# Kernel optimization log

Hardware: AMD Instinct MI355X
Metric: run time of the kernel (lower is better)

## Reference

```python
import jax, jax.numpy as jnp
import numpy as np

T, DM = 2048, 2048
H, KV, D = 16, 2, 128
E, I_MOE, I_SH = 16, 768, 768
TOP_K, N_GROUP, TOPK_GROUP = 4, 4, 2
ROPE_THETA = 1e6
EPS = 1e-5
ROUTED_SCALE = 1.0


def rmsnorm(x, w):
    v = jnp.mean(x * x, axis=-1, keepdims=True)
    return x * jax.lax.rsqrt(v + EPS) * w


def apply_rope(x, pos):
    # partial rotary: first D//2 dims rotated (neox style), rest passthrough
    rd = D // 2
    half = rd // 2
    inv = 1.0 / (ROPE_THETA ** (jnp.arange(0, rd, 2, dtype=jnp.float32) / rd))
    freqs = pos.astype(jnp.float32)[:, None] * inv  # [T, half]
    cos = jnp.cos(freqs)[:, None, :]
    sin = jnp.sin(freqs)[:, None, :]
    x1, x2 = x[..., :half], x[..., half:rd]
    rot = jnp.concatenate([x1 * cos - x2 * sin, x2 * cos + x1 * sin], axis=-1)
    return jnp.concatenate([rot, x[..., rd:]], axis=-1)


def mlp(x, wgu, wd):
    g, u = jnp.split(x @ wgu, 2, axis=-1)
    return (jax.nn.silu(g) * u) @ wd


def attention(x, pos, w_qkv, b_qkv, w_o, q_norm_w, k_norm_w):
    qkv = x @ w_qkv + b_qkv
    q, k, v = jnp.split(qkv, [H * D, H * D + KV * D], axis=-1)
    q = rmsnorm(q.reshape(T, H, D), q_norm_w)
    k = rmsnorm(k.reshape(T, KV, D), k_norm_w)
    v = v.reshape(T, KV, D)
    q = apply_rope(q, pos)
    k = apply_rope(k, pos)
    rep = H // KV
    k = jnp.repeat(k, rep, axis=1)
    v = jnp.repeat(v, rep, axis=1)
    scores = jnp.einsum('thd,shd->hts', q, k) * (D ** -0.5)
    causal = pos[:, None] >= pos[None, :]
    scores = jnp.where(causal[None], scores, jnp.finfo(scores.dtype).min)
    p = jax.nn.softmax(scores, axis=-1)
    o = jnp.einsum('hts,shd->thd', p, v).reshape(T, H * D)
    return o @ w_o


def moe(x, gate_w, gate_bias, shared_wgu, shared_wd, expert_wgu, expert_wd):
    # sigmoid grouped top-k routing with e_score_correction_bias (DeepSeek/GLM style)
    logits = x.astype(jnp.float32) @ gate_w
    scores = jax.nn.sigmoid(logits)
    sb = scores + gate_bias
    g = sb.reshape(T, N_GROUP, E // N_GROUP)
    group_scores = jnp.sum(jax.lax.top_k(g, 2)[0], axis=-1)  # [T, n_group]
    _, gi = jax.lax.top_k(group_scores, TOPK_GROUP)
    gmask = jnp.zeros((T, N_GROUP)).at[jnp.arange(T)[:, None], gi].set(1.0)
    emask = jnp.repeat(gmask, E // N_GROUP, axis=1)
    masked = jnp.where(emask > 0, sb, -jnp.inf)
    _, idx = jax.lax.top_k(masked, TOP_K)  # [T, top_k]
    w = jnp.take_along_axis(scores, idx, axis=1)
    w = w / jnp.sum(w, axis=1, keepdims=True)  # renormalize (norm_topk_prob)
    cw = jnp.zeros((T, E)).at[jnp.arange(T)[:, None], idx].add(w)  # dense combine weights
    gu = jnp.einsum('td,edi->tei', x, expert_wgu)  # [T, E, 2I]
    gt, ut = jnp.split(gu, 2, axis=-1)
    act = jax.nn.silu(gt) * ut * cw[:, :, None]
    routed = jnp.einsum('tei,eid->td', act, expert_wd)
    shared = mlp(x, shared_wgu, shared_wd)
    return routed * ROUTED_SCALE + shared


def setup_inputs() -> dict:
    key = jax.random.key(0)
    ks = jax.random.split(key, 12)
    s = 0.02
    return {
        'positions': jnp.arange(T, dtype=jnp.int32),
        'hidden_states': jax.random.normal(ks[0], (T, DM), jnp.float32),
        'residual': jax.random.normal(ks[1], (T, DM), jnp.float32),
        'ln1_w': jnp.ones((DM,), jnp.float32),
        'ln2_w': jnp.ones((DM,), jnp.float32),
        'w_qkv': jax.random.normal(ks[2], (DM, (H + 2 * KV) * D), jnp.float32) * s,
        'b_qkv': jnp.zeros(((H + 2 * KV) * D,), jnp.float32),
        'w_o': jax.random.normal(ks[3], (H * D, DM), jnp.float32) * s,
        'q_norm_w': jnp.ones((D,), jnp.float32),
        'k_norm_w': jnp.ones((D,), jnp.float32),
        'gate_w': jax.random.normal(ks[4], (DM, E), jnp.float32) * s,
        'gate_bias': jax.random.normal(ks[5], (E,), jnp.float32) * 0.1,
        'shared_wgu': jax.random.normal(ks[6], (DM, 2 * I_SH), jnp.float32) * s,
        'shared_wd': jax.random.normal(ks[7], (I_SH, DM), jnp.float32) * s,
        'expert_wgu': jax.random.normal(ks[8], (E, DM, 2 * I_MOE), jnp.float32) * s,
        'expert_wd': jax.random.normal(ks[9], (E, I_MOE, DM), jnp.float32) * s,
    }


def reference(positions, hidden_states, residual, ln1_w, ln2_w, w_qkv, b_qkv, w_o,
              q_norm_w, k_norm_w, gate_w, gate_bias, shared_wgu, shared_wd,
              expert_wgu, expert_wd):
    # fused add + RMSNorm (residual is not None path)
    residual = hidden_states + residual
    h = rmsnorm(residual, ln1_w)
    h = attention(h, positions, w_qkv, b_qkv, w_o, q_norm_w, k_norm_w)
    residual = h + residual
    h = rmsnorm(residual, ln2_w)
    h = moe(h, gate_w, gate_bias, shared_wgu, shared_wd, expert_wgu, expert_wd)
    return h, residual
```

## Files before the change

### kernel.cpp

```cpp
#include <hip/hip_runtime.h>
#include <stdint.h>
#include <math.h>

#define T_ 2048
#define DM 2048
#define NH 16
#define NKV 2
#define HD 128
#define QKVN 2560
#define NE 16
#define IM 768
#define ISH 768
#define MAXROWS 10240
#define ROWS_ALL 12288
#define NBLK 136
#define SM_SCALE 0.08838834764831845f

typedef __attribute__((ext_vector_type(8))) short short8;
typedef __attribute__((ext_vector_type(4))) float f32x4;

__device__ __forceinline__ float bf2f(unsigned short u){ return __uint_as_float(((unsigned int)u)<<16); }
__device__ __forceinline__ unsigned short f2bf(float f){
  unsigned int u = __float_as_uint(f);
  return (unsigned short)((u + 0x7FFFu + ((u>>16)&1u)) >> 16);
}
__device__ __forceinline__ void split2(float x, unsigned short& hi, unsigned short& lo){
  hi = f2bf(x);
  lo = f2bf(x - bf2f(hi));
}

__device__ __forceinline__ void gload16(const void* g, void* l){
  __builtin_amdgcn_global_load_lds((const __attribute__((address_space(1))) unsigned int*)g,
                                   (__attribute__((address_space(3))) unsigned int*)l, 16, 0, 0);
}

__device__ __forceinline__ int xcd_swz(int bid, int nwg){
  int q = nwg >> 3, r = nwg & 7, x = bid & 7, p = bid >> 3;
  return (x < r ? x*(q+1) : r*(q+1) + (x-r)*q) + p;
}

#define BAR()    asm volatile("s_barrier" ::: "memory")
#define VW(N)    asm volatile("s_waitcnt vmcnt(" #N ")" ::: "memory")
#define LW0()    do{ asm volatile("s_waitcnt lgkmcnt(0)" ::: "memory"); __builtin_amdgcn_sched_barrier(0); }while(0)

template<bool ILV>
__global__ void k_tconv(const float* __restrict__ src, unsigned short* __restrict__ dst,
                        const float* __restrict__ srcS, unsigned short* __restrict__ dstS,
                        int R, int C, size_t sS, size_t sD){
  int z = blockIdx.z;
  if (srcS && z == gridDim.z-1){ src = srcS; dst = dstS; }
  else { src += (size_t)z * sS; dst += (size_t)z * sD; }
  __shared__ float tile[64*65];
  int tid = threadIdx.x;
  int r0 = blockIdx.y*64, c0 = blockIdx.x*64;
  int lr = tid>>4, lc = (tid&15)*4;
  #pragma unroll
  for (int j=0;j<4;j++){
    int row = j*16 + lr;
    float4 v = *(const float4*)&src[(size_t)(r0+row)*C + c0 + lc];
    float* t = &tile[row*65 + lc];
    t[0]=v.x; t[1]=v.y; t[2]=v.z; t[3]=v.w;
  }
  __syncthreads();
  #pragma unroll
  for (int jj=0;jj<2;jj++){
    int slot = jj*256 + tid;
    int c = slot>>3, ro = (slot&7)*8;
    int cg = c0 + c;
    int cd = cg;
    if (ILV){ int b = cg>>3, inner = cg&7; cd = (b<96 ? b*16 : (b-96)*16+8) + inner; }
    short8 o;
    #pragma unroll
    for (int k=0;k<8;k++) o[k] = (short)f2bf(tile[(ro+k)*65 + c]);
    *(short8*)&dst[(size_t)cd*R + r0 + ro] = o;
  }
}

__global__ void k_tconv2(const float* __restrict__ src, unsigned short* __restrict__ dhi,
                         unsigned short* __restrict__ dlo, int R, int C){
  __shared__ float tile[64*65];
  int tid = threadIdx.x;
  int r0 = blockIdx.y*64, c0 = blockIdx.x*64;
  int lr = tid>>4, lc = (tid&15)*4;
  #pragma unroll
  for (int j=0;j<4;j++){
    int row = j*16 + lr;
    float4 v = *(const float4*)&src[(size_t)(r0+row)*C + c0 + lc];
    float* t = &tile[row*65 + lc];
    t[0]=v.x; t[1]=v.y; t[2]=v.z; t[3]=v.w;
  }
  __syncthreads();
  #pragma unroll
  for (int jj=0;jj<2;jj++){
    int slot = jj*256 + tid;
    int c = slot>>3, ro = (slot&7)*8;
    short8 oh, ol;
    #pragma unroll
    for (int k=0;k<8;k++){
      unsigned short h_, l_;
      split2(tile[(ro+k)*65 + c], h_, l_);
      oh[k] = (short)h_; ol[k] = (short)l_;
    }
    size_t o = (size_t)(c0+c)*R + r0 + ro;
    *(short8*)&dhi[o] = oh;
    *(short8*)&dlo[o] = ol;
  }
}

template<bool ROUTE>
__global__ void k_add_rmsnorm(const float* __restrict__ a, const float* __restrict__ b,
                              const float* __restrict__ w, float* __restrict__ resout,
                              unsigned short* __restrict__ ohi, unsigned short* __restrict__ olo,
                              unsigned short* __restrict__ obf,
                              const float* __restrict__ gw, const float* __restrict__ gbias,
                              int* __restrict__ idx4, float* __restrict__ w4){
  int t = blockIdx.x, tid = threadIdx.x;
  const float4* a4 = (const float4*)(a + (size_t)t*DM);
  const float4* b4 = (const float4*)(b + (size_t)t*DM);
  float4 va = a4[tid], vb = b4[tid];
  float4 wa = a4[tid+256], wb = b4[tid+256];
  float4 v0, v1;
  v0.x=va.x+vb.x; v0.y=va.y+vb.y; v0.z=va.z+vb.z; v0.w=va.w+vb.w;
  v1.x=wa.x+wb.x; v1.y=wa.y+wb.y; v1.z=wa.z+wb.z; v1.w=wa.w+wb.w;
  float s = v0.x*v0.x+v0.y*v0.y+v0.z*v0.z+v0.w*v0.w
          + v1.x*v1.x+v1.y*v1.y+v1.z*v1.z+v1.w*v1.w;
  #pragma unroll
  for (int o=32;o;o>>=1) s += __shfl_xor(s,o);
  __shared__ float sm[4];
  if ((tid&63)==0) sm[tid>>6]=s;
  __syncthreads();
  s = sm[0]+sm[1]+sm[2]+sm[3];
  float rs = rsqrtf(s*(1.f/(float)DM) + 1e-5f);
  ((float4*)(resout + (size_t)t*DM))[tid] = v0;
  ((float4*)(resout + (size_t)t*DM))[tid+256] = v1;
  const float4* w4p_ = (const float4*)w;
  float4 w0 = w4p_[tid], w1 = w4p_[tid+256];
  float n[8] = { v0.x*rs*w0.x, v0.y*rs*w0.y, v0.z*rs*w0.z, v0.w*rs*w0.w,
                 v1.x*rs*w1.x, v1.y*rs*w1.y, v1.z*rs*w1.z, v1.w*rs*w1.w };
  if (ohi){
    ushort4 h0,h1,l0,l1;
    split2(n[0],h0.x,l0.x); split2(n[1],h0.y,l0.y); split2(n[2],h0.z,l0.z); split2(n[3],h0.w,l0.w);
    split2(n[4],h1.x,l1.x); split2(n[5],h1.y,l1.y); split2(n[6],h1.z,l1.z); split2(n[7],h1.w,l1.w);
    ((ushort4*)(ohi + (size_t)t*DM))[tid] = h0;
    ((ushort4*)(ohi + (size_t)t*DM))[tid+256] = h1;
    ((ushort4*)(olo + (size_t)t*DM))[tid] = l0;
    ((ushort4*)(olo + (size_t)t*DM))[tid+256] = l1;
  }
  if (obf){
    ushort4 o0 = make_ushort4(f2bf(n[0]),f2bf(n[1]),f2bf(n[2]),f2bf(n[3]));
    ushort4 o1 = make_ushort4(f2bf(n[4]),f2bf(n[5]),f2bf(n[6]),f2bf(n[7]));
    ((ushort4*)(obf + (size_t)t*DM))[tid] = o0;
    ((ushort4*)(obf + (size_t)t*DM))[tid+256] = o1;
  }
  if constexpr (ROUTE){
    __shared__ float xrow[DM];
    __shared__ float red[16][17];
    #pragma unroll
    for (int jj=0;jj<4;jj++) xrow[4*tid+jj] = n[jj];
    #pragma unroll
    for (int jj=0;jj<4;jj++) xrow[1024+4*tid+jj] = n[4+jj];
    __syncthreads();
    int e = tid & 15, grp = tid >> 4;
    float part = 0.f;
    #pragma unroll 8
    for (int c = grp; c < DM; c += 16)
      part += xrow[c] * gw[(size_t)c*16 + e];
    red[grp][e] = part;
    __syncthreads();
    if (tid==0){
      float sc[16], sb[16];
      for (int ee=0;ee<16;ee++){
        float lg = 0.f;
        for (int g2=0;g2<16;g2++) lg += red[g2][ee];
        sc[ee] = 1.f/(1.f+expf(-lg));
        sb[ee] = sc[ee] + gbias[ee];
      }
      float gs[4];
      for (int g=0;g<4;g++){
        float m1=-3.4e38f, m2=-3.4e38f;
        for (int j=0;j<4;j++){
          float v = sb[g*4+j];
          if (v>m1){ m2=m1; m1=v; } else if (v>m2) m2=v;
        }
        gs[g]=m1+m2;
      }
      int g1=0; for (int g=1;g<4;g++) if (gs[g]>gs[g1]) g1=g;
      int g2=-1; for (int g=0;g<4;g++){ if (g==g1) continue; if (g2<0 || gs[g]>gs[g2]) g2=g; }
      float msk[16];
      for (int ee=0;ee<16;ee++){ int g=ee>>2; msk[ee] = (g==g1||g==g2)? sb[ee] : -3.4e38f; }
      int id[4]; float wv[4]; float wsum=0.f;
      for (int s2=0;s2<4;s2++){
        int bb=0; float bv=-3.5e38f;
        for (int ee=0;ee<16;ee++) if (msk[ee]>bv){ bv=msk[ee]; bb=ee; }
        id[s2]=bb; wv[s2]=sc[bb]; wsum+=sc[bb]; msk[bb]=-3.5e38f;
      }
      float invs = 1.f/wsum;
      for (int s2=0;s2<4;s2++){
        idx4[t*4+s2]=id[s2];
        w4[t*4+s2]=wv[s2]*invs;
      }
    }
  }
}

template<bool GATHER, bool ACT>
__global__ __launch_bounds__(256) void k_gemm2(
    const unsigned short* __restrict__ A, const unsigned short* __restrict__ Be,
    const unsigned short* __restrict__ Bsh, unsigned short* __restrict__ C,
    int K, int lda, int ldb, int ldc,
    const int* __restrict__ offs, size_t sBe, const int* __restrict__ tok){
  int nx = gridDim.x;
  int nwg = nx * gridDim.y;
  int wid_ = xcd_swz(blockIdx.x + nx*blockIdx.y, nwg);
  int tN = wid_ % nx, tM = wid_ / nx;
  int rb = tM*128;
  if (rb >= offs[17]) return;
  const unsigned short* B;
  if (rb >= offs[16]) B = Bsh;
  else {
    int e=0;
    for (; e<15; ++e) if (offs[e+1] > rb) break;
    B = Be + (size_t)e*sBe;
  }
  __shared__ __align__(16) unsigned short As[2][4096];
  __shared__ __align__(16) unsigned short Bs[2][4096];
  int tid = threadIdx.x, lane = tid & 63, wwid = tid >> 6;
  int wr = wwid >> 1, wc = wwid & 1;
  const unsigned short* Bb = B + (size_t)tN*128*ldb;

  const unsigned short* Asrc0;
  const unsigned short* Asrc1;
  int r0s = tid>>2, r1s = r0s + 64;
  {
    if (GATHER){
      Asrc0 = A + (size_t)tok[rb + r0s]*lda;
      Asrc1 = A + (size_t)tok[rb + r1s]*lda;
    } else {
      Asrc0 = A + (size_t)(rb + r0s)*lda;
      Asrc1 = A + (size_t)(rb + r1s)*lda;
    }
  }
  int kc = tid&3;
  int sw = (r0s>>1)&3;
  int kcS = (kc ^ sw)*8;

  f32x4 acc[4][4];
  #pragma unroll
  for (int m=0;m<4;m++)
    #pragma unroll
    for (int n=0;n<4;n++) acc[m][n] = (f32x4){0.f,0.f,0.f,0.f};

  auto STAGE = [&](int b, int k0){
    gload16(Asrc0 + k0 + kcS, As[b] + (size_t)tid*8);
    gload16(Asrc1 + k0 + kcS, As[b] + (size_t)(256+tid)*8);
    gload16(Bb + (size_t)r0s*ldb + k0 + kcS, Bs[b] + (size_t)tid*8);
    gload16(Bb + (size_t)r1s*ldb + k0 + kcS, Bs[b] + (size_t)(256+tid)*8);
  };

  int nt = K >> 5, L = nt - 1;
  STAGE(0, 0);
  if (L >= 1) STAGE(1, 32);
  int i15 = lane & 15, g = lane >> 4;
  for (int i=0; i<nt; ++i){
    int cur = i & 1;
    if (i < L) { VW(4); } else { VW(0); }
    BAR();
    short8 af[4], bfr[4];
    #pragma unroll
    for (int m=0;m<4;m++){
      int row = wr*64 + m*16 + i15;
      int geff = g ^ ((row>>1)&3);
      af[m] = *(const short8*)(As[cur] + row*32 + geff*8);
    }
    #pragma unroll
    for (int n=0;n<4;n++){
      int row = wc*64 + n*16 + i15;
      int geff = g ^ ((row>>1)&3);
      bfr[n] = *(const short8*)(Bs[cur] + row*32 + geff*8);
    }
    LW0();
    BAR();
    if (i + 2 <= L) STAGE(cur, (i+2)*32);
    __builtin_amdgcn_s_setprio(1);
    #pragma unroll
    for (int m=0;m<4;m++)
      #pragma unroll
      for (int n=0;n<4;n++)
        acc[m][n] = __builtin_amdgcn_mfma_f32_16x16x32_bf16(af[m], bfr[n], acc[m][n], 0,0,0);
    __builtin_amdgcn_s_setprio(0);
  }

  if (ACT){
    int rbase = rb + wr*64, cb = tN*128 + wc*64;
    #pragma unroll
    for (int m=0;m<4;m++){
      int r0 = rbase + m*16 + ((lane>>4)<<2);
      #pragma unroll
      for (int n=0;n<4;n++){
        int f = ((cb + n*16)>>1) + (lane&7);
        #pragma unroll
        for (int r=0;r<4;r++){
          float v = acc[m][n][r];
          float vp = __shfl_xor(v, 8);
          if (!(lane&8)){
            float gg = v;
            float a = gg/(1.f+__expf(-gg))*vp;
            C[(size_t)(r0+r)*ldc + f] = f2bf(a);
          }
        }
      }
    }
  } else {
    int rbase = rb + wr*64, cb = tN*128 + wc*64;
    #pragma unroll
    for (int m=0;m<4;m++){
      int r0 = rbase + m*16 + ((lane>>4)<<2);
      #pragma unroll
      for (int n=0;n<4;n++){
        int c = cb + n*16 + (lane&15);
        #pragma unroll
        for (int r=0;r<4;r++) C[(size_t)(r0+r)*ldc + c] = f2bf(acc[m][n][r]);
      }
    }
  }
}

__global__ __launch_bounds__(256) void k_gemm_hp(
    const unsigned short* __restrict__ Ah, const unsigned short* __restrict__ Al,
    const unsigned short* __restrict__ Bh, const unsigned short* __restrict__ Bl,
    float* __restrict__ Cf,
    int K, int lda, int ldb, int ldc){
  int nx = gridDim.x, nwg = nx*gridDim.y;
  int w = xcd_swz(blockIdx.x + nx*blockIdx.y, nwg);
  int tN = w % nx, tM = w / nx;

  __shared__ __align__(16) unsigned short AsH[2][4096], AsL[2][4096];
  __shared__ __align__(16) unsigned short BsH[2][4096], BsL[2][4096];
  int tid = threadIdx.x, lane = tid & 63, wid = tid >> 6;
  int wr = wid >> 1, wc = wid & 1;
  const unsigned short* Abh = Ah + (size_t)tM*128*lda;
  const unsigned short* Abl = Al + (size_t)tM*128*lda;
  const unsigned short* Bbh = Bh + (size_t)tN*128*ldb;
  const unsigned short* Bbl = Bl + (size_t)tN*128*ldb;

  f32x4 acc[4][4];
  #pragma unroll
  for (int m=0;m<4;m++)
    #pragma unroll
    for (int n=0;n<4;n++) acc[m][n] = (f32x4){0.f,0.f,0.f,0.f};

  auto STAGE = [&](int b, int k0){
    #pragma unroll
    for (int j=0;j<2;j++){
      int cb = j*256 + tid;
      int row = cb>>2, kc = cb&3;
      int kcS = (kc ^ ((row>>1)&3))*8;
      size_t go = (size_t)row*lda + k0 + kcS;
      gload16(Abh + go, AsH[b] + (size_t)cb*8);
      gload16(Abl + go, AsL[b] + (size_t)cb*8);
      size_t bo = (size_t)row*ldb + k0 + kcS;
      gload16(Bbh + bo, BsH[b] + (size_t)cb*8);
      gload16(Bbl + bo, BsL[b] + (size_t)cb*8);
    }
  };

  int nt = K >> 5, L = nt - 1;
  STAGE(0, 0);
  if (L >= 1) STAGE(1, 32);
  int i15 = lane & 15, g = lane >> 4;
  for (int i=0; i<nt; ++i){
    int cur = i & 1;
    if (i < L) { VW(8); } else { VW(0); }
    BAR();
    short8 afh[4], afl[4], bfh[4], bfl[4];
    #pragma unroll
    for (int m=0;m<4;m++){
      int row = wr*64 + m*16 + i15;
      int ro = row*32 + (g ^ ((row>>1)&3))*8;
      afh[m] = *(const short8*)(AsH[cur] + ro);
      afl[m] = *(const short8*)(AsL[cur] + ro);
    }
    #pragma unroll
    for (int n=0;n<4;n++){
      int row = wc*64 + n*16 + i15;
      int ro = row*32 + (g ^ ((row>>1)&3))*8;
      bfh[n] = *(const short8*)(BsH[cur] + ro);
      bfl[n] = *(const short8*)(BsL[cur] + ro);
    }
    LW0();
    BAR();
    if (i + 2 <= L) STAGE(cur, (i+2)*32);
    __builtin_amdgcn_s_setprio(1);
    #pragma unroll
    for (int m=0;m<4;m++)
      #pragma unroll
      for (int n=0;n<4;n++){
        acc[m][n] = __builtin_amdgcn_mfma_f32_16x16x32_bf16(afh[m], bfh[n], acc[m][n], 0,0,0);
        acc[m][n] = __builtin_amdgcn_mfma_f32_16x16x32_bf16(afh[m], bfl[n], acc[m][n], 0,0,0);
        acc[m][n] = __builtin_amdgcn_mfma_f32_16x16x32_bf16(afl[m], bfh[n], acc[m][n], 0,0,0);
      }
    __builtin_amdgcn_s_setprio(0);
  }

  int rb = tM*128 + wr*64, cb = tN*128 + wc*64;
  #pragma unroll
  for (int m=0;m<4;m++){
    int r0 = rb + m*16 + ((lane>>4)<<2);
    #pragma unroll
    for (int n=0;n<4;n++){
      int c = cb + n*16 + (lane&15);
      #pragma unroll
      for (int r=0;r<4;r++) Cf[(size_t)(r0+r)*ldc + c] = acc[m][n][r];
    }
  }
}

__global__ __launch_bounds__(256) void k_qk_pers(
    const unsigned short* __restrict__ Qh, const unsigned short* __restrict__ Ql,
    const unsigned short* __restrict__ Kh, const unsigned short* __restrict__ Kl,
    float* __restrict__ Sp){
  int tM = blockIdx.x, z = blockIdx.y;
  int kvh = z >> 3;
  size_t tri = (size_t)tM*(tM+1)/2;
  const int ldq = NH*HD, ldk = NKV*HD;
  const unsigned short* Qbh = Qh + (size_t)(tM*128)*ldq + (size_t)z*HD;
  const unsigned short* Qbl = Ql + (size_t)(tM*128)*ldq + (size_t)z*HD;
  const unsigned short* Kbh = Kh + (size_t)kvh*HD;
  const unsigned short* Kbl = Kl + (size_t)kvh*HD;

  __shared__ __align__(16) unsigned short QsH[16384], QsL[16384];
  __shared__ __align__(16) unsigned short BsH[2][4096], BsL[2][4096];

  int tid = threadIdx.x, lane = tid & 63, wid = tid >> 6;
  int wr = wid >> 1, wc = wid & 1;
  int i15 = lane & 15, g = lane >> 4;

  #pragma unroll
  for (int j=0;j<8;j++){
    int gi = j*256 + tid;
    int chunk = gi >> 9;
    int row = (gi >> 2) & 127;
    int gg = gi & 3;
    int col = chunk*32 + (gg ^ ((row>>1)&3))*8;
    gload16(Qbh + (size_t)row*ldq + col, QsH + (size_t)gi*8);
    gload16(Qbl + (size_t)row*ldq + col, QsL + (size_t)gi*8);
  }

  auto BSTAGE = [&](int b, int ci){
    int tn = ci >> 2, c = ci & 3;
    const unsigned short* sh = Kbh + (size_t)(tn*128)*ldk;
    const unsigned short* sl = Kbl + (size_t)(tn*128)*ldk;
    #pragma unroll
    for (int j=0;j<2;j++){
      int gi = j*256 + tid;
      int row = gi >> 2, gg = gi & 3;
      int col = c*32 + (gg ^ ((row>>1)&3))*8;
      gload16(sh + (size_t)row*ldk + col, BsH[b] + (size_t)gi*8);
      gload16(sl + (size_t)row*ldk + col, BsL[b] + (size_t)gi*8);
    }
  };

  f32x4 acc[4][4];
  #pragma unroll
  for (int m=0;m<4;m++)
    #pragma unroll
    for (int n=0;n<4;n++) acc[m][n] = (f32x4){0.f,0.f,0.f,0.f};

  int NC = (tM+1)*4;
  BSTAGE(0, 0);
  BSTAGE(1, 1);
  for (int ci=0; ci<NC; ++ci){
    int cur = ci & 1, c = ci & 3, tn = ci >> 2;
    if (ci < NC-1) { VW(4); } else { VW(0); }
    BAR();
    short8 afh[4], afl[4], bfh[4], bfl[4];
    #pragma unroll
    for (int m=0;m<4;m++){
      int row = wr*64 + m*16 + i15;
      int ro = c*4096 + row*32 + (g ^ ((row>>1)&3))*8;
      afh[m] = *(const short8*)(QsH + ro);
      afl[m] = *(const short8*)(QsL + ro);
    }
    #pragma unroll
    for (int n=0;n<4;n++){
      int row = wc*64 + n*16 + i15;
      int ro = row*32 + (g ^ ((row>>1)&3))*8;
      bfh[n] = *(const short8*)(BsH[cur] + ro);
      bfl[n] = *(const short8*)(BsL[cur] + ro);
    }
    LW0();
    BAR();
    if (ci + 2 < NC) BSTAGE(cur, ci+2);
    __builtin_amdgcn_s_setprio(1);
    #pragma unroll
    for (int m=0;m<4;m++)
      #pragma unroll
      for (int n=0;n<4;n++){
        acc[m][n] = __builtin_amdgcn_mfma_f32_16x16x32_bf16(afh[m], bfh[n], acc[m][n], 0,0,0);
        acc[m][n] = __builtin_amdgcn_mfma_f32_16x16x32_bf16(afh[m], bfl[n], acc[m][n], 0,0,0);
        acc[m][n] = __builtin_amdgcn_mfma_f32_16x16x32_bf16(afl[m], bfh[n], acc[m][n], 0,0,0);
      }
    __builtin_amdgcn_s_setprio(0);
    if (c == 3){
      float* Cb = Sp + ((size_t)z*NBLK + tri + tn)*16384;
      #pragma unroll
      for (int m=0;m<4;m++){
        int r0 = wr*64 + m*16 + (g<<2);
        #pragma unroll
        for (int n=0;n<4;n++){
          int ccol = wc*64 + n*16 + i15;
          #pragma unroll
          for (int r=0;r<4;r++) Cb[(size_t)(r0+r)*128 + ccol] = acc[m][n][r];
        }
      }
      #pragma unroll
      for (int m=0;m<4;m++)
        #pragma unroll
        for (int n=0;n<4;n++) acc[m][n] = (f32x4){0.f,0.f,0.f,0.f};
    }
  }
}

__global__ void k_softmax_ml(float* __restrict__ Sp, float* __restrict__ mlb){
  int t = blockIdx.x, h = blockIdx.y, tid = threadIdx.x;
  int tM = t>>7, tr = t&127;
  size_t base = ((size_t)h*NBLK + (size_t)tM*(tM+1)/2)*16384 + (size_t)tr*128;
  int nv = t+1, kc = (tM+1)<<7;
  __shared__ float sm[4];
  float rv[8];
  #pragma unroll
  for (int j=0;j<8;j++){
    int s = tid + j*256;
    rv[j] = (s<nv) ? Sp[base + (size_t)(s>>7)*16384 + (s&127)]*SM_SCALE : -1e30f;
  }
  float m = rv[0];
  #pragma unroll
  for (int j=1;j<8;j++) m = fmaxf(m, rv[j]);
  #pragma unroll
  for (int o=32;o;o>>=1) m = fmaxf(m, __shfl_xor(m,o));
  if ((tid&63)==0) sm[tid>>6]=m;
  __syncthreads();
  m = fmaxf(fmaxf(sm[0],sm[1]),fmaxf(sm[2],sm[3]));
  __syncthreads();
  float sum = 0.f;
  #pragma unroll
  for (int j=0;j<8;j++) sum += __expf(rv[j]-m);
  #pragma unroll
  for (int o=32;o;o>>=1) sum += __shfl_xor(sum,o);
  if ((tid&63)==0) sm[tid>>6]=sum;
  __syncthreads();
  sum = sm[0]+sm[1]+sm[2]+sm[3];
  if (tid==0) mlb[(size_t)h*T_ + t] = m + logf(sum);
  for (int s = nv + tid; s < kc; s += 256)
    Sp[base + (size_t)(s>>7)*16384 + (s&127)] = -1e30f;
}

__global__ __launch_bounds__(256) void k_pv_hp(
    const float* __restrict__ Sp, const float* __restrict__ mlb,
    const unsigned short* __restrict__ Vh, const unsigned short* __restrict__ Vl,
    float* __restrict__ part){
  int c = blockIdx.x, tM = blockIdx.y, z = blockIdx.z;
  int kbeg = c*512;
  int kend = min((tM+1)*128, (c+1)*512);
  if (kbeg >= kend) return;
  size_t tri = (size_t)tM*(tM+1)/2;
  const float* Ab = Sp + ((size_t)z*NBLK + tri)*16384;
  const unsigned short* Bbh = Vh + (size_t)(z>>3)*HD*T_;
  const unsigned short* Bbl = Vl + (size_t)(z>>3)*HD*T_;

  __shared__ __align__(16) float Asf[2][4096];
  __shared__ __align__(16) unsigned short BsH[2][4096], BsL[2][4096];
  int tid = threadIdx.x, lane = tid & 63, wid = tid >> 6;
  int wr = wid >> 1, wc = wid & 1;
  int i15 = lane & 15, g2 = (lane>>4)*2;

  float mrow[4];
  #pragma unroll
  for (int m=0;m<4;m++)
    mrow[m] = mlb[(size_t)z*T_ + tM*128 + wr*64 + m*16 + i15];

  int r0s = tid>>2, r1s = r0s + 64;
  int kcB = ((tid&3) ^ ((r0s>>1)&3))*8;
  int rowA = tid>>3, gA = tid&7;

  f32x4 acc[4][4];
  #pragma unroll
  for (int m=0;m<4;m++)
    #pragma unroll
    for (int n=0;n<4;n++) acc[m][n] = (f32x4){0.f,0.f,0.f,0.f};

  auto STAGE = [&](int b, int k0){
    #pragma unroll
    for (int j=0;j<4;j++){
      int r = j*32 + rowA;
      int gS = gA ^ (r & 7);
      size_t ga = (size_t)(k0>>7)*16384 + (size_t)r*128 + (k0&127) + gS*4;
      gload16(Ab + ga, Asf[b] + ((size_t)j*256 + tid)*4);
    }
    size_t bo0 = (size_t)r0s*T_ + k0 + kcB;
    size_t bo1 = (size_t)r1s*T_ + k0 + kcB;
    gload16(Bbh + bo0, BsH[b] + (size_t)tid*8);
    gload16(Bbh + bo1, BsH[b] + (size_t)(256+tid)*8);
    gload16(Bbl + bo0, BsL[b] + (size_t)tid*8);
    gload16(Bbl + bo1, BsL[b] + (size_t)(256+tid)*8);
  };

  int nt = (kend - kbeg) >> 5, L = nt - 1;
  STAGE(0, kbeg);
  if (L >= 1) STAGE(1, kbeg + 32);
  for (int i=0; i<nt; ++i){
    int cur = i & 1;
    if (i < L) { VW(8); } else { VW(0); }
    BAR();
    short8 afh[4], afl[4], bfh[4], bfl[4];
    #pragma unroll
    for (int m=0;m<4;m++){
      int r = wr*64 + m*16 + i15;
      int s0 = r*8 + ((g2  ) ^ (r&7));
      int s1 = r*8 + ((g2+1) ^ (r&7));
      f32x4 a0 = *(const f32x4*)(Asf[cur] + s0*4);
      f32x4 a1 = *(const f32x4*)(Asf[cur] + s1*4);
      float pv[8] = {a0[0],a0[1],a0[2],a0[3],a1[0],a1[1],a1[2],a1[3]};
      short8 h8, l8;
      #pragma unroll
      for (int j=0;j<8;j++){
        float p = __expf(pv[j]*SM_SCALE - mrow[m]);
        unsigned short hh, ll; split2(p, hh, ll);
        h8[j] = (short)hh; l8[j] = (short)ll;
      }
      afh[m] = h8; afl[m] = l8;
    }
    #pragma unroll
    for (int n=0;n<4;n++){
      int row = wc*64 + n*16 + i15;
      int ro = row*32 + ((lane>>4) ^ ((row>>1)&3))*8;
      bfh[n] = *(const short8*)(BsH[cur] + ro);
      bfl[n] = *(const short8*)(BsL[cur] + ro);
    }
    LW0();
    BAR();
    if (i + 2 <= L) STAGE(cur, kbeg + (i+2)*32);
    __builtin_amdgcn_s_setprio(1);
    #pragma unroll
    for (int m=0;m<4;m++)
      #pragma unroll
      for (int n=0;n<4;n++){
        acc[m][n] = __builtin_amdgcn_mfma_f32_16x16x32_bf16(afh[m], bfh[n], acc[m][n], 0,0,0);
        acc[m][n] = __builtin_amdgcn_mfma_f32_16x16x32_bf16(afh[m], bfl[n], acc[m][n], 0,0,0);
        acc[m][n] = __builtin_amdgcn_mfma_f32_16x16x32_bf16(afl[m], bfh[n], acc[m][n], 0,0,0);
      }
    __builtin_amdgcn_s_setprio(0);
  }

  float* Cb = part + (size_t)c*T_*DM + (size_t)tM*128*DM + (size_t)z*HD;
  #pragma unroll
  for (int m=0;m<4;m++){
    int r0 = wr*64 + m*16 + ((lane>>4)<<2);
    #pragma unroll
    for (int n=0;n<4;n++){
      int ccol = wc*64 + n*16 + (lane&15);
      #pragma unroll
      for (int r=0;r<4;r++) Cb[(size_t)(r0+r)*DM + ccol] = acc[m][n][r];
    }
  }
}

__global__ void k_pv_reduce(const float* __restrict__ part,
                            unsigned short* __restrict__ aoh, unsigned short* __restrict__ aol){
  int t = blockIdx.x, tid = threadIdx.x;
  int nc = ((t>>7) + 4) >> 2;
  #pragma unroll
  for (int half=0; half<2; ++half){
    int idx = tid + half*256;
    float4 s = ((const float4*)(part + (size_t)t*DM))[idx];
    for (int c=1; c<nc; ++c){
      float4 v = ((const float4*)(part + (size_t)c*T_*DM + (size_t)t*DM))[idx];
      s.x+=v.x; s.y+=v.y; s.z+=v.z; s.w+=v.w;
    }
    ushort4 h_, l_;
    split2(s.x,h_.x,l_.x); split2(s.y,h_.y,l_.y); split2(s.z,h_.z,l_.z); split2(s.w,h_.w,l_.w);
    ((ushort4*)(aoh + (size_t)t*DM))[idx] = h_;
    ((ushort4*)(aol + (size_t)t*DM))[idx] = l_;
  }
}

__global__ void k_qkv_post_hp(const float* __restrict__ qkv, const float* __restrict__ bias,
                              const float* __restrict__ qnw, const float* __restrict__ knw,
                              const int* __restrict__ pos_,
                              unsigned short* __restrict__ qhi, unsigned short* __restrict__ qlo,
                              unsigned short* __restrict__ khi, unsigned short* __restrict__ klo,
                              unsigned short* __restrict__ vThi, unsigned short* __restrict__ vTlo){
  int t = blockIdx.x;
  int half = threadIdx.x >> 7;
  int d = threadIdx.x & 127;
  int wseg = (threadIdx.x >> 6) & 1;
  float posf = (float)pos_[t];
  __shared__ float buf[2][128];
  __shared__ float ssum[2][2];
  __shared__ float inv_sh[32];
  if (threadIdx.x < 32)
    inv_sh[threadIdx.x] = (float)pow(1000000.0, -(double)threadIdx.x/32.0);
  __syncthreads();
  for (int it=0; it<10; ++it){
    int seg = it*2 + half;
    float x = qkv[(size_t)t*QKVN + seg*128 + d] + bias[seg*128 + d];
    float p = x*x;
    #pragma unroll
    for (int o=32;o;o>>=1) p += __shfl_xor(p,o);
    if ((threadIdx.x&63)==0) ssum[half][wseg] = p;
    __syncthreads();
    float rs = rsqrtf((ssum[half][0]+ssum[half][1])*(1.f/128.f) + 1e-5f);
    float w = (seg<16) ? qnw[d] : ((seg<18) ? knw[d] : 1.f);
    float nv = x*rs*w;
    buf[half][d] = nv;
    __syncthreads();
    float outv = (seg<18) ? nv : x;
    if (seg < 18 && d < 64){
      int i = d & 31;
      float ang = posf * inv_sh[i];
      float sn, cs; sincosf(ang, &sn, &cs);
      if (d < 32) outv = nv*cs - buf[half][d+32]*sn;
      else        outv = nv*cs + buf[half][d-32]*sn;
    }
    unsigned short h_, l_; split2(outv, h_, l_);
    if (seg < 16){ size_t o = ((size_t)t*NH + seg)*HD + d; qhi[o]=h_; qlo[o]=l_; }
    else if (seg < 18){ size_t o = ((size_t)t*NKV + (seg-16))*HD + d; khi[o]=h_; klo[o]=l_; }
    else { size_t o = ((size_t)(seg-18)*HD + d)*T_ + t; vThi[o]=h_; vTlo[o]=l_; }
    __syncthreads();
  }
}

__global__ void k_offplace(const int* __restrict__ idx4, int* __restrict__ offs,
                           int* __restrict__ rrow, int* __restrict__ tok){
  __shared__ int hist[16];
  __shared__ int hoff[16];
  __shared__ int fill[16];
  int tid = threadIdx.x;
  if (tid < 16) hist[tid] = 0;
  __syncthreads();
  for (int i = tid; i < ROWS_ALL; i += 256) tok[i] = 0;
  for (int i = tid; i < T_*4; i += 256)
    atomicAdd(&hist[idx4[i]], 1);
  __syncthreads();
  if (tid == 0){
    int o = 0;
    for (int e=0;e<16;e++){ hoff[e]=o; offs[e]=o; o += ((hist[e]+127)>>7)<<7; }
    offs[16]=o;
    offs[17]=o + T_;
  }
  if (tid < 16) fill[tid] = 0;
  __syncthreads();
  int off16 = offs[16];
  for (int t = tid; t < T_; t += 256){
    #pragma unroll
    for (int s=0;s<4;s++){
      int e = idx4[t*4+s];
      int p = atomicAdd(&fill[e],1);
      int r = hoff[e]+p;
      rrow[t*4+s]=r;
      tok[r]=t;
    }
    tok[off16+t] = t;
  }
}

__global__ void k_combine(const unsigned short* __restrict__ eout,
                          const int* __restrict__ rrow, const float* __restrict__ w4,
                          const int* __restrict__ offs, float* __restrict__ outh){
  int t = blockIdx.x;
  int rs = offs[16] + t;
  int r0=rrow[t*4+0], r1=rrow[t*4+1], r2=rrow[t*4+2], r3=rrow[t*4+3];
  float w0=w4[t*4+0], w1=w4[t*4+1], w2=w4[t*4+2], w3=w4[t*4+3];
  for (int d=threadIdx.x; d<DM; d+=256){
    float v = bf2f(eout[(size_t)rs*DM+d])
            + w0*bf2f(eout[(size_t)r0*DM+d]) + w1*bf2f(eout[(size_t)r1*DM+d])
            + w2*bf2f(eout[(size_t)r2*DM+d]) + w3*bf2f(eout[(size_t)r3*DM+d]);
    outh[(size_t)t*DM+d] = v;
  }
}

extern "C" void kernel_launch(void* const* d_in, const int* in_sizes, int n_in,
                              void* d_out, int out_size, void* d_ws, size_t ws_size,
                              hipStream_t stream){
  const int*   positions = (const int*)d_in[0];
  const float* hidden    = (const float*)d_in[1];
  const float* residual  = (const float*)d_in[2];
  const float* ln1       = (const float*)d_in[3];
  const float* ln2       = (const float*)d_in[4];
  const float* w_qkv     = (const float*)d_in[5];
  const float* b_qkv     = (const float*)d_in[6];
  const float* w_o       = (const float*)d_in[7];
  const float* qnw       = (const float*)d_in[8];
  const float* knw       = (const float*)d_in[9];
  const float* gate_w    = (const float*)d_in[10];
  const float* gate_b    = (const float*)d_in[11];
  const float* sh_wgu    = (const float*)d_in[12];
  const float* sh_wd     = (const float*)d_in[13];
  const float* e_wgu     = (const float*)d_in[14];
  const float* e_wd      = (const float*)d_in[15];
  float* out_h   = (float*)d_out;
  float* out_res = (float*)d_out + (size_t)T_*DM;

  char* ws = (char*)d_ws;
  size_t off = 0;
  auto alloc = [&](size_t b){ size_t r = off; off += (b + 255) & ~(size_t)255; return r; };

  size_t o_h2b  = alloc((size_t)T_*DM*2);
  size_t o_idx  = alloc((size_t)T_*4*4);
  size_t o_w4   = alloc((size_t)T_*4*4);
  size_t o_offs = alloc(72);
  size_t o_rrow = alloc((size_t)T_*4*4);
  size_t o_tok  = alloc((size_t)ROWS_ALL*4);

  size_t U0 = off;
  size_t a = U0;
  auto allocA = [&](size_t b){ size_t r = a; a += (b + 255) & ~(size_t)255; return r; };
  size_t o_h1h  = allocA((size_t)T_*DM*2);
  size_t o_h1l  = allocA((size_t)T_*DM*2);
  size_t o_wqh  = allocA((size_t)QKVN*DM*2);
  size_t o_wql  = allocA((size_t)QKVN*DM*2);
  size_t o_qkvf = allocA((size_t)T_*QKVN*4);
  size_t o_qh   = allocA((size_t)T_*NH*HD*2);
  size_t o_ql   = allocA((size_t)T_*NH*HD*2);
  size_t o_kh   = allocA((size_t)T_*NKV*HD*2);
  size_t o_kl   = allocA((size_t)T_*NKV*HD*2);
  size_t o_vth  = allocA((size_t)NKV*HD*T_*2);
  size_t o_vtl  = allocA((size_t)NKV*HD*T_*2);
  size_t o_woh  = allocA((size_t)DM*DM*2);
  size_t o_wol  = allocA((size_t)DM*DM*2);
  size_t o_aoh  = allocA((size_t)T_*DM*2);
  size_t o_aol  = allocA((size_t)T_*DM*2);
  size_t o_attnP= allocA((size_t)T_*DM*4);
  size_t o_mlb  = allocA((size_t)NH*T_*4);
  size_t o_Sp   = allocA((size_t)NH*NBLK*16384*4);
  size_t o_pvp  = allocA((size_t)4*T_*DM*4);
  size_t b_ = U0;
  auto allocB = [&](size_t b){ size_t r = b_; b_ += (b + 255) & ~(size_t)255; return r; };
  size_t o_ewgu = allocB((size_t)NE*2*IM*DM*2);
  size_t o_ewd  = allocB((size_t)NE*DM*IM*2);
  size_t o_shgu = allocB((size_t)2*ISH*DM*2);
  size_t o_shwd = allocB((size_t)DM*ISH*2);
  size_t o_actx = allocB((size_t)ROWS_ALL*IM*2);
  size_t o_eout = allocB((size_t)ROWS_ALL*DM*2);

  unsigned short* h2b   = (unsigned short*)(ws+o_h2b);
  int*   idx4  = (int*)(ws+o_idx);
  float* w4p   = (float*)(ws+o_w4);
  int*   offs  = (int*)(ws+o_offs);
  int*   rrow  = (int*)(ws+o_rrow);
  int*   tok   = (int*)(ws+o_tok);
  unsigned short* h1h = (unsigned short*)(ws+o_h1h);
  unsigned short* h1l = (unsigned short*)(ws+o_h1l);
  unsigned short* wqh = (unsigned short*)(ws+o_wqh);
  unsigned short* wql = (unsigned short*)(ws+o_wql);
  float*          qkvf= (float*)(ws+o_qkvf);
  unsigned short* qh  = (unsigned short*)(ws+o_qh);
  unsigned short* ql  = (unsigned short*)(ws+o_ql);
  unsigned short* kh  = (unsigned short*)(ws+o_kh);
  unsigned short* kl  = (unsigned short*)(ws+o_kl);
  unsigned short* vth = (unsigned short*)(ws+o_vth);
  unsigned short* vtl = (unsigned short*)(ws+o_vtl);
  unsigned short* woh = (unsigned short*)(ws+o_woh);
  unsigned short* wol = (unsigned short*)(ws+o_wol);
  unsigned short* aoh = (unsigned short*)(ws+o_aoh);
  unsigned short* aol = (unsigned short*)(ws+o_aol);
  float*          attnP=(float*)(ws+o_attnP);
  float*          mlb = (float*)(ws+o_mlb);
  float*          Sp  = (float*)(ws+o_Sp);
  float*          pvpart = (float*)(ws+o_pvp);
  unsigned short* ewguT=(unsigned short*)(ws+o_ewgu);
  unsigned short* ewdT = (unsigned short*)(ws+o_ewd);
  unsigned short* shguT=(unsigned short*)(ws+o_shgu);
  unsigned short* shwdT=(unsigned short*)(ws+o_shwd);
  unsigned short* actx= (unsigned short*)(ws+o_actx);
  unsigned short* eout= (unsigned short*)(ws+o_eout);

  k_tconv2<<<dim3(QKVN/64, DM/64, 1),256,0,stream>>>(w_qkv, wqh, wql, DM, QKVN);
  k_tconv2<<<dim3(DM/64, DM/64, 1),256,0,stream>>>(w_o, woh, wol, DM, DM);

  k_add_rmsnorm<false><<<T_,256,0,stream>>>(hidden, residual, ln1, out_res, h1h, h1l, nullptr,
                                            nullptr, nullptr, nullptr, nullptr);

  k_gemm_hp<<<dim3(QKVN/128,T_/128,1),256,0,stream>>>(
      h1h, h1l, wqh, wql, qkvf, DM, DM, DM, QKVN);
  k_qkv_post_hp<<<T_,256,0,stream>>>(qkvf, b_qkv, qnw, knw, positions, qh, ql, kh, kl, vth, vtl);

  k_qk_pers<<<dim3(T_/128,NH),256,0,stream>>>(qh, ql, kh, kl, Sp);
  k_softmax_ml<<<dim3(T_,NH),256,0,stream>>>(Sp, mlb);
  k_pv_hp<<<dim3(4,T_/128,NH),256,0,stream>>>(Sp, mlb, vth, vtl, pvpart);
  k_pv_reduce<<<T_,256,0,stream>>>(pvpart, aoh, aol);
  k_gemm_hp<<<dim3(DM/128,T_/128,1),256,0,stream>>>(
      aoh, aol, woh, wol, attnP, DM, DM, DM, DM);

  k_add_rmsnorm<true><<<T_,256,0,stream>>>(attnP, out_res, ln2, out_res, nullptr, nullptr, h2b,
                                           gate_w, gate_b, idx4, w4p);

  k_offplace<<<1,256,0,stream>>>(idx4, offs, rrow, tok);

  k_tconv<true ><<<dim3(2*IM/64, DM/64, NE+1),256,0,stream>>>(
      e_wgu, ewguT, sh_wgu, shguT, DM, 2*IM, (size_t)DM*2*IM, (size_t)2*IM*DM);
  k_tconv<false><<<dim3(DM/64, IM/64, NE+1),256,0,stream>>>(
      e_wd,  ewdT,  sh_wd,  shwdT, IM, DM,   (size_t)IM*DM,   (size_t)DM*IM);

  k_gemm2<true, true ><<<dim3(2*IM/128, ROWS_ALL/128, 1),256,0,stream>>>(
      h2b, ewguT, shguT, actx, DM, DM, DM, IM, offs, (size_t)2*IM*DM, tok);
  k_gemm2<false, false><<<dim3(DM/128, ROWS_ALL/128, 1),256,0,stream>>>(
      actx, ewdT, shwdT, eout, IM, IM, IM, DM, offs, (size_t)DM*IM, nullptr);

  k_combine<<<T_,256,0,stream>>>(eout, rrow, w4p, offs, out_h);
}
```

Measured before the change: 737.4 us.

## Drop separate softmax pass; fold normalization into PV kernel and reduce

```diff
diff --git a/kernel.cpp b/kernel.cpp
--- a/kernel.cpp
+++ b/kernel.cpp
@@ -76,8 +76,16 @@
   }
 }
 
-__global__ void k_tconv2(const float* __restrict__ src, unsigned short* __restrict__ dhi,
-                         unsigned short* __restrict__ dlo, int R, int C){
+__global__ void k_tconv2(const float* __restrict__ srcA, unsigned short* __restrict__ dhiA,
+                         unsigned short* __restrict__ dloA,
+                         const float* __restrict__ srcB, unsigned short* __restrict__ dhiB,
+                         unsigned short* __restrict__ dloB){
+  const float* src; unsigned short* dhi; unsigned short* dlo; int R, C;
+  if (blockIdx.z == 0){ src = srcA; dhi = dhiA; dlo = dloA; R = DM; C = QKVN; }
+  else {
+    if (blockIdx.x >= DM/64) return;
+    src = srcB; dhi = dhiB; dlo = dloB; R = DM; C = DM;
+  }
   __shared__ float tile[64*65];
   int tid = threadIdx.x;
   int r0 = blockIdx.y*64, c0 = blockIdx.x*64;
@@ -521,48 +529,15 @@
   }
 }
 
-__global__ void k_softmax_ml(float* __restrict__ Sp, float* __restrict__ mlb){
-  int t = blockIdx.x, h = blockIdx.y, tid = threadIdx.x;
-  int tM = t>>7, tr = t&127;
-  size_t base = ((size_t)h*NBLK + (size_t)tM*(tM+1)/2)*16384 + (size_t)tr*128;
-  int nv = t+1, kc = (tM+1)<<7;
-  __shared__ float sm[4];
-  float rv[8];
-  #pragma unroll
-  for (int j=0;j<8;j++){
-    int s = tid + j*256;
-    rv[j] = (s<nv) ? Sp[base + (size_t)(s>>7)*16384 + (s&127)]*SM_SCALE : -1e30f;
-  }
-  float m = rv[0];
-  #pragma unroll
-  for (int j=1;j<8;j++) m = fmaxf(m, rv[j]);
-  #pragma unroll
-  for (int o=32;o;o>>=1) m = fmaxf(m, __shfl_xor(m,o));
-  if ((tid&63)==0) sm[tid>>6]=m;
-  __syncthreads();
-  m = fmaxf(fmaxf(sm[0],sm[1]),fmaxf(sm[2],sm[3]));
-  __syncthreads();
-  float sum = 0.f;
-  #pragma unroll
-  for (int j=0;j<8;j++) sum += __expf(rv[j]-m);
-  #pragma unroll
-  for (int o=32;o;o>>=1) sum += __shfl_xor(sum,o);
-  if ((tid&63)==0) sm[tid>>6]=sum;
-  __syncthreads();
-  sum = sm[0]+sm[1]+sm[2]+sm[3];
-  if (tid==0) mlb[(size_t)h*T_ + t] = m + logf(sum);
-  for (int s = nv + tid; s < kc; s += 256)
-    Sp[base + (size_t)(s>>7)*16384 + (s&127)] = -1e30f;
-}
-
 __global__ __launch_bounds__(256) void k_pv_hp(
-    const float* __restrict__ Sp, const float* __restrict__ mlb,
+    const float* __restrict__ Sp,
     const unsigned short* __restrict__ Vh, const unsigned short* __restrict__ Vl,
-    float* __restrict__ part){
+    float* __restrict__ part, float* __restrict__ rsums){
   int c = blockIdx.x, tM = blockIdx.y, z = blockIdx.z;
   int kbeg = c*512;
   int kend = min((tM+1)*128, (c+1)*512);
   if (kbeg >= kend) return;
+  int tMk = tM*128;
   size_t tri = (size_t)tM*(tM+1)/2;
   const float* Ab = Sp + ((size_t)z*NBLK + tri)*16384;
   const unsigned short* Bbh = Vh + (size_t)(z>>3)*HD*T_;
@@ -574,11 +549,6 @@
   int wr = wid >> 1, wc = wid & 1;
   int i15 = lane & 15, g2 = (lane>>4)*2;
 
-  float mrow[4];
-  #pragma unroll
-  for (int m=0;m<4;m++)
-    mrow[m] = mlb[(size_t)z*T_ + tM*128 + wr*64 + m*16 + i15];
-
   int r0s = tid>>2, r1s = r0s + 64;
   int kcB = ((tid&3) ^ ((r0s>>1)&3))*8;
   int rowA = tid>>3, gA = tid&7;
@@ -588,6 +558,7 @@
   for (int m=0;m<4;m++)
     #pragma unroll
     for (int n=0;n<4;n++) acc[m][n] = (f32x4){0.f,0.f,0.f,0.f};
+  float rsum[4] = {0.f,0.f,0.f,0.f};
 
   auto STAGE = [&](int b, int k0){
     #pragma unroll
@@ -610,8 +581,10 @@
   if (L >= 1) STAGE(1, kbeg + 32);
   for (int i=0; i<nt; ++i){
     int cur = i & 1;
+    int k0 = kbeg + i*32;
     if (i < L) { VW(8); } else { VW(0); }
     BAR();
+    int diag = (k0 >= tMk);
     short8 afh[4], afl[4], bfh[4], bfl[4];
     #pragma unroll
     for (int m=0;m<4;m++){
@@ -621,10 +594,19 @@
       f32x4 a0 = *(const f32x4*)(Asf[cur] + s0*4);
       f32x4 a1 = *(const f32x4*)(Asf[cur] + s1*4);
       float pv[8] = {a0[0],a0[1],a0[2],a0[3],a1[0],a1[1],a1[2],a1[3]};
+      if (diag){
+        int kb = k0 & 127;
+        #pragma unroll
+        for (int j=0;j<8;j++){
+          int kl = kb + ((j<4) ? g2*4 + j : (g2+1)*4 + (j-4));
+          if (kl > r) pv[j] = -3.0e38f;
+        }
+      }
       short8 h8, l8;
       #pragma unroll
       for (int j=0;j<8;j++){
-        float p = __expf(pv[j]*SM_SCALE - mrow[m]);
+        float p = __expf(pv[j]*SM_SCALE);
+        rsum[m] += p;
         unsigned short hh, ll; split2(p, hh, ll);
         h8[j] = (short)hh; l8[j] = (short)ll;
       }
@@ -652,7 +634,16 @@
     __builtin_amdgcn_s_setprio(0);
   }
 
-  float* Cb = part + (size_t)c*T_*DM + (size_t)tM*128*DM + (size_t)z*HD;
+  #pragma unroll
+  for (int m=0;m<4;m++){
+    float v = rsum[m];
+    v += __shfl_xor(v, 16);
+    v += __shfl_xor(v, 32);
+    if ((lane>>4)==0 && wc==0)
+      rsums[((size_t)c*NH + z)*T_ + tMk + wr*64 + m*16 + i15] = v;
+  }
+
+  float* Cb = part + (size_t)c*T_*DM + (size_t)tMk*DM + (size_t)z*HD;
   #pragma unroll
   for (int m=0;m<4;m++){
     int r0 = wr*64 + m*16 + ((lane>>4)<<2);
@@ -665,18 +656,23 @@
   }
 }
 
-__global__ void k_pv_reduce(const float* __restrict__ part,
+__global__ void k_pv_reduce(const float* __restrict__ part, const float* __restrict__ rsums,
                             unsigned short* __restrict__ aoh, unsigned short* __restrict__ aol){
   int t = blockIdx.x, tid = threadIdx.x;
   int nc = ((t>>7) + 4) >> 2;
   #pragma unroll
   for (int half=0; half<2; ++half){
     int idx = tid + half*256;
+    int z = idx >> 5;
+    float tot = 0.f;
+    for (int c=0; c<nc; ++c) tot += rsums[((size_t)c*NH + z)*T_ + t];
+    float inv = 1.f / tot;
     float4 s = ((const float4*)(part + (size_t)t*DM))[idx];
     for (int c=1; c<nc; ++c){
       float4 v = ((const float4*)(part + (size_t)c*T_*DM + (size_t)t*DM))[idx];
       s.x+=v.x; s.y+=v.y; s.z+=v.z; s.w+=v.w;
     }
+    s.x*=inv; s.y*=inv; s.z*=inv; s.w*=inv;
     ushort4 h_, l_;
     split2(s.x,h_.x,l_.x); split2(s.y,h_.y,l_.y); split2(s.z,h_.z,l_.z); split2(s.w,h_.w,l_.w);
     ((ushort4*)(aoh + (size_t)t*DM))[idx] = h_;
@@ -831,7 +827,7 @@
   size_t o_aoh  = allocA((size_t)T_*DM*2);
   size_t o_aol  = allocA((size_t)T_*DM*2);
   size_t o_attnP= allocA((size_t)T_*DM*4);
-  size_t o_mlb  = allocA((size_t)NH*T_*4);
+  size_t o_rsum = allocA((size_t)4*NH*T_*4);
   size_t o_Sp   = allocA((size_t)NH*NBLK*16384*4);
   size_t o_pvp  = allocA((size_t)4*T_*DM*4);
   size_t b_ = U0;
@@ -865,7 +861,7 @@
   unsigned short* aoh = (unsigned short*)(ws+o_aoh);
   unsigned short* aol = (unsigned short*)(ws+o_aol);
   float*          attnP=(float*)(ws+o_attnP);
-  float*          mlb = (float*)(ws+o_mlb);
+  float*          rsums=(float*)(ws+o_rsum);
   float*          Sp  = (float*)(ws+o_Sp);
   float*          pvpart = (float*)(ws+o_pvp);
   unsigned short* ewguT=(unsigned short*)(ws+o_ewgu);
@@ -875,8 +871,7 @@
   unsigned short* actx= (unsigned short*)(ws+o_actx);
   unsigned short* eout= (unsigned short*)(ws+o_eout);
 
-  k_tconv2<<<dim3(QKVN/64, DM/64, 1),256,0,stream>>>(w_qkv, wqh, wql, DM, QKVN);
-  k_tconv2<<<dim3(DM/64, DM/64, 1),256,0,stream>>>(w_o, woh, wol, DM, DM);
+  k_tconv2<<<dim3(QKVN/64, DM/64, 2),256,0,stream>>>(w_qkv, wqh, wql, w_o, woh, wol);
 
   k_add_rmsnorm<false><<<T_,256,0,stream>>>(hidden, residual, ln1, out_res, h1h, h1l, nullptr,
                                             nullptr, nullptr, nullptr, nullptr);
@@ -886,9 +881,8 @@
   k_qkv_post_hp<<<T_,256,0,stream>>>(qkvf, b_qkv, qnw, knw, positions, qh, ql, kh, kl, vth, vtl);
 
   k_qk_pers<<<dim3(T_/128,NH),256,0,stream>>>(qh, ql, kh, kl, Sp);
-  k_softmax_ml<<<dim3(T_,NH),256,0,stream>>>(Sp, mlb);
-  k_pv_hp<<<dim3(4,T_/128,NH),256,0,stream>>>(Sp, mlb, vth, vtl, pvpart);
-  k_pv_reduce<<<T_,256,0,stream>>>(pvpart, aoh, aol);
+  k_pv_hp<<<dim3(4,T_/128,NH),256,0,stream>>>(Sp, vth, vtl, pvpart, rsums);
+  k_pv_reduce<<<T_,256,0,stream>>>(pvpart, rsums, aoh, aol);
   k_gemm_hp<<<dim3(DM/128,T_/128,1),256,0,stream>>>(
       aoh, aol, woh, wol, attnP, DM, DM, DM, DM);
 
```

After: 700.3 us. 1.05x faster.
